# Performance work log

Hardware: AMD Instinct MI355X
Metric: run time of the kernel (lower is better)

Reference implementation:

```python
import jax, jax.numpy as jnp
import numpy as np

D_MODEL = 768
NUM_HEADS = 12
HEAD_DIM = D_MODEL // NUM_HEADS
BATCH = 1
SEQ = 4096


def setup_inputs() -> dict:
    key = jax.random.key(0)
    ks = jax.random.split(key, 11)
    s = 0.02
    return {
        "q": jax.random.normal(ks[0], (BATCH, SEQ, D_MODEL), jnp.float32),
        "k": jax.random.normal(ks[1], (BATCH, SEQ, D_MODEL), jnp.float32),
        "v": jax.random.normal(ks[2], (BATCH, SEQ, D_MODEL), jnp.float32),
        "Wq": jax.random.normal(ks[3], (D_MODEL, D_MODEL), jnp.float32) * s,
        "bq": jnp.zeros((D_MODEL,), jnp.float32),
        "Wk": jax.random.normal(ks[4], (D_MODEL, D_MODEL), jnp.float32) * s,
        "bk": jnp.zeros((D_MODEL,), jnp.float32),
        "Wv": jax.random.normal(ks[5], (D_MODEL, D_MODEL), jnp.float32) * s,
        "bv": jnp.zeros((D_MODEL,), jnp.float32),
        "Wo": jax.random.normal(ks[6], (D_MODEL, D_MODEL), jnp.float32) * s,
        "bo": jnp.zeros((D_MODEL,), jnp.float32),
    }


def reference(q, k, v, Wq, bq, Wk, bk, Wv, bv, Wo, bo):
    B, S, D = q.shape
    H, Hd = NUM_HEADS, HEAD_DIM
    # linear projections (torch Linear: x @ W.T + b)
    qh = (q @ Wq.T + bq).reshape(B, S, H, Hd).transpose(0, 2, 1, 3)  # [B,H,S,Hd]
    kh = (k @ Wk.T + bk).reshape(B, S, H, Hd).transpose(0, 2, 1, 3)
    vh = (v @ Wv.T + bv).reshape(B, S, H, Hd).transpose(0, 2, 1, 3)
    scale = 1.0 / jnp.sqrt(jnp.asarray(Hd, qh.dtype))
    scores = jnp.einsum("bhsd,bhtd->bhst", qh, kh) * scale  # [B,H,S,S]
    weights = jax.nn.softmax(scores, axis=-1)
    attn = jnp.einsum("bhst,bhtd->bhsd", weights, vh)  # [B,H,S,Hd]
    attn = attn.transpose(0, 2, 1, 3).reshape(B, S, D)
    return attn @ Wo.T + bo
```

## Files before the change

### kernel.cpp

```cpp
#include <hip/hip_runtime.h>

#define S_LEN 4096
#define DMODEL 768
#define NHEAD 12
#define HD 64

typedef __bf16 bf16x8 __attribute__((ext_vector_type(8)));
typedef __bf16 bf16x4 __attribute__((ext_vector_type(4)));
typedef float f32x4 __attribute__((ext_vector_type(4)));
typedef float f32x16 __attribute__((ext_vector_type(16)));
typedef unsigned short u16x8 __attribute__((ext_vector_type(8)));
typedef unsigned short u16x4 __attribute__((ext_vector_type(4)));
typedef _Float16 f16x4 __attribute__((ext_vector_type(4)));

#if __has_builtin(__builtin_amdgcn_exp2f)
#define EXP2F(x) __builtin_amdgcn_exp2f(x)
#else
#define EXP2F(x) exp2f(x)
#endif

#define MFMA32(a, b, c) __builtin_amdgcn_mfma_f32_32x32x16_bf16(a, b, c, 0, 0, 0)

__device__ __forceinline__ unsigned short f2bf(float f) {
  unsigned int u = __float_as_uint(f);
  u += 0x7fffu + ((u >> 16) & 1u);
  return (unsigned short)(u >> 16);
}

__device__ __forceinline__ void gload_lds16(const void* g, void* l) {
  __builtin_amdgcn_global_load_lds(
      (__attribute__((address_space(1))) void*)g,
      (__attribute__((address_space(3))) void*)l, 16, 0, 0);
}

struct CvtArgs {
  const float* src[7];
  unsigned short* dst[7];
  int n[7];
};

__global__ __launch_bounds__(256) void cvt_kernel(CvtArgs a) {
  const int seg = blockIdx.y;
  const int n = a.n[seg];
  const int i = (blockIdx.x * 256 + threadIdx.x) * 8;
  if (i >= n) return;
  const float* s = a.src[seg] + i;
  u16x8 o;
#pragma unroll
  for (int j = 0; j < 8; ++j) o[j] = f2bf(s[j]);
  *reinterpret_cast<u16x8*>(a.dst[seg] + i) = o;
}

struct QkvArgs {
  const unsigned short* A[3];
  const unsigned short* W[3];
  const float* bias[3];
  unsigned short* dst[3];
  float scale[3];
};

__global__ __launch_bounds__(256) void qkv_gemm(QkvArgs a) {
  __shared__ unsigned char lds[32768];
  const int z = blockIdx.z;
  const unsigned short* __restrict__ A = a.A[z];
  const unsigned short* __restrict__ B = a.W[z];
  const float* __restrict__ bias = a.bias[z];
  unsigned short* __restrict__ dst = a.dst[z];
  const float scale = a.scale[z];

  const int tid = threadIdx.x;
  const int lane = tid & 63;
  const int w = tid >> 6;
  const int wr = w >> 1, wc = w & 1;
  const int c = lane & 15, g = lane >> 4;
  const int m0 = blockIdx.x * 128;
  const int n0 = blockIdx.y * 128;

  f32x4 acc[4][4] = {};

  for (int kt = 0; kt < DMODEL / 64; ++kt) {
#pragma unroll
    for (int p = 0; p < 4; ++p) {
      const int te = p * 256 + tid;
      const int row = te >> 3;
      const int sb = ((te & 7) * 16) ^ ((row & 7) << 4);
      gload_lds16(A + (size_t)(m0 + row) * DMODEL + kt * 64 + (sb >> 1), &lds[te * 16]);
      gload_lds16(B + (size_t)(n0 + row) * DMODEL + kt * 64 + (sb >> 1), &lds[16384 + te * 16]);
    }
    __syncthreads();

    bf16x8 af[4][2], bfr[4][2];
#pragma unroll
    for (int mb = 0; mb < 4; ++mb)
#pragma unroll
      for (int ks = 0; ks < 2; ++ks) {
        const int row = wr * 64 + mb * 16 + c;
        const int byte = (ks * 64 + g * 16) ^ ((row & 7) << 4);
        af[mb][ks] = *reinterpret_cast<const bf16x8*>(&lds[row * 128 + byte]);
      }
#pragma unroll
    for (int nb = 0; nb < 4; ++nb)
#pragma unroll
      for (int ks = 0; ks < 2; ++ks) {
        const int row = wc * 64 + nb * 16 + c;
        const int byte = (ks * 64 + g * 16) ^ ((row & 7) << 4);
        bfr[nb][ks] = *reinterpret_cast<const bf16x8*>(&lds[16384 + row * 128 + byte]);
      }
    __builtin_amdgcn_s_setprio(1);
#pragma unroll
    for (int ks = 0; ks < 2; ++ks)
#pragma unroll
      for (int mb = 0; mb < 4; ++mb)
#pragma unroll
        for (int nb = 0; nb < 4; ++nb)
          acc[mb][nb] = __builtin_amdgcn_mfma_f32_16x16x32_bf16(
              af[mb][ks], bfr[nb][ks], acc[mb][nb], 0, 0, 0);
    __builtin_amdgcn_s_setprio(0);
    __syncthreads();
  }

#pragma unroll
  for (int mb = 0; mb < 4; ++mb) {
#pragma unroll
    for (int nb = 0; nb < 4; ++nb) {
      const int n = n0 + wc * 64 + nb * 16 + c;
      const float bv = bias[n];
#pragma unroll
      for (int r = 0; r < 4; ++r) {
        const int m = m0 + wr * 64 + mb * 16 + g * 4 + r;
        const float v = (acc[mb][nb][r] + bv) * scale;
        const int hh = n >> 6, hd = n & 63;
        if (z != 2) {
          dst[((size_t)hh * S_LEN + m) * HD + hd] = f2bf(v);
        } else {
          const int mp = (m & ~12) | ((m & 4) << 1) | ((m & 8) >> 1);
          dst[((size_t)hh * HD + hd) * S_LEN + mp] = f2bf(v);
        }
      }
    }
  }
}

__global__ __launch_bounds__(256) void gemm_out(
    const unsigned short* __restrict__ A, const unsigned short* __restrict__ B,
    const float* __restrict__ bias, float* __restrict__ dst) {
  __shared__ unsigned char lds[32768];
  const int tid = threadIdx.x;
  const int lane = tid & 63;
  const int w = tid >> 6;
  const int wr = w >> 1, wc = w & 1;
  const int c = lane & 15, g = lane >> 4;
  const int m0 = blockIdx.x * 128;
  const int n0 = blockIdx.y * 128;

  f32x4 acc[4][4] = {};

  for (int kt = 0; kt < DMODEL / 64; ++kt) {
#pragma unroll
    for (int p = 0; p < 4; ++p) {
      const int te = p * 256 + tid;
      const int row = te >> 3;
      const int sb = ((te & 7) * 16) ^ ((row & 7) << 4);
      gload_lds16(A + (size_t)(m0 + row) * DMODEL + kt * 64 + (sb >> 1), &lds[te * 16]);
      gload_lds16(B + (size_t)(n0 + row) * DMODEL + kt * 64 + (sb >> 1), &lds[16384 + te * 16]);
    }
    __syncthreads();

    bf16x8 af[4][2], bfr[4][2];
#pragma unroll
    for (int mb = 0; mb < 4; ++mb)
#pragma unroll
      for (int ks = 0; ks < 2; ++ks) {
        const int row = wr * 64 + mb * 16 + c;
        const int byte = (ks * 64 + g * 16) ^ ((row & 7) << 4);
        af[mb][ks] = *reinterpret_cast<const bf16x8*>(&lds[row * 128 + byte]);
      }
#pragma unroll
    for (int nb = 0; nb < 4; ++nb)
#pragma unroll
      for (int ks = 0; ks < 2; ++ks) {
        const int row = wc * 64 + nb * 16 + c;
        const int byte = (ks * 64 + g * 16) ^ ((row & 7) << 4);
        bfr[nb][ks] = *reinterpret_cast<const bf16x8*>(&lds[16384 + row * 128 + byte]);
      }
    __builtin_amdgcn_s_setprio(1);
#pragma unroll
    for (int ks = 0; ks < 2; ++ks)
#pragma unroll
      for (int mb = 0; mb < 4; ++mb)
#pragma unroll
        for (int nb = 0; nb < 4; ++nb)
          acc[mb][nb] = __builtin_amdgcn_mfma_f32_16x16x32_bf16(
              af[mb][ks], bfr[nb][ks], acc[mb][nb], 0, 0, 0);
    __builtin_amdgcn_s_setprio(0);
    __syncthreads();
  }

#pragma unroll
  for (int mb = 0; mb < 4; ++mb)
#pragma unroll
    for (int nb = 0; nb < 4; ++nb) {
      const int n = n0 + wc * 64 + nb * 16 + c;
      const float bv = bias[n];
#pragma unroll
      for (int r = 0; r < 4; ++r) {
        const int m = m0 + wr * 64 + mb * 16 + g * 4 + r;
        dst[(size_t)m * DMODEL + n] = acc[mb][nb][r] + bv;
      }
    }
}

__global__ __launch_bounds__(256) void attn_kernel(
    const unsigned short* __restrict__ qh,
    const unsigned short* __restrict__ kh,
    const unsigned short* __restrict__ vtp,
    _Float16* __restrict__ pacc,
    float* __restrict__ prs) {
  __shared__ unsigned char lds[32768];
  const int tid = threadIdx.x;
  const int lane = tid & 63;
  const int w = tid >> 6;
  const int c5 = lane & 31;
  const int h2 = lane >> 5;
  const int hh = blockIdx.y;
  const int split = blockIdx.z;
  const int qw = blockIdx.x * 128 + w * 32;
  const int kv0 = split * (S_LEN / 2);
  const int NKT = (S_LEN / 2) / 64;

  bf16x8 qa[4];
#pragma unroll
  for (int ks = 0; ks < 4; ++ks)
    qa[ks] = *reinterpret_cast<const bf16x8*>(
        qh + ((size_t)hh * S_LEN + qw + c5) * HD + ks * 16 + h2 * 8);

  const int r63 = tid & 63;
  const int kch = tid >> 6;
  const unsigned short* ksrc =
      kh + ((size_t)hh * S_LEN + kv0 + r63) * HD + kch * 8;
  const unsigned short* vsrc =
      vtp + ((size_t)hh * HD + r63) * S_LEN + kv0 + kch * 8;
  const int dL = tid * 16;

  gload_lds16(ksrc, &lds[dL]);
  gload_lds16(ksrc + 32, &lds[4096 + dL]);
  gload_lds16(vsrc, &lds[8192 + dL]);
  gload_lds16(vsrc + 32, &lds[12288 + dL]);
  ksrc += 64 * HD;
  vsrc += 64;

  f32x16 accO[2] = {};
  float rs0 = 0.f, rs1 = 0.f, rs2 = 0.f, rs3 = 0.f;

  auto compute = [&](const unsigned char* Kb, const unsigned char* Vb) {
    f32x16 s0 = {}, s1 = {};
    __builtin_amdgcn_s_setprio(1);
#pragma unroll
    for (int ks = 0; ks < 4; ++ks) {
      const unsigned char* kbase = Kb + (ks * 2 + h2) * 1024 + c5 * 16;
      const bf16x8 k0 = *reinterpret_cast<const bf16x8*>(kbase);
      const bf16x8 k1 = *reinterpret_cast<const bf16x8*>(kbase + 512);
      s0 = MFMA32(k0, qa[ks], s0);
      s1 = MFMA32(k1, qa[ks], s1);
    }
    __builtin_amdgcn_s_setprio(0);

    bf16x8 p00, p01, p10, p11;
#pragma unroll
    for (int r = 0; r < 8; ++r) {
      const float e0 = EXP2F(s0[r]);
      const float e1 = EXP2F(s0[8 + r]);
      const float e2 = EXP2F(s1[r]);
      const float e3 = EXP2F(s1[8 + r]);
      rs0 += e0; rs1 += e1; rs2 += e2; rs3 += e3;
      p00[r] = (__bf16)e0;
      p01[r] = (__bf16)e1;
      p10[r] = (__bf16)e2;
      p11[r] = (__bf16)e3;
    }

    __builtin_amdgcn_s_setprio(1);
#pragma unroll
    for (int t = 0; t < 2; ++t)
#pragma unroll
      for (int ss = 0; ss < 2; ++ss) {
        const bf16x8 pb = t ? (ss ? p11 : p10) : (ss ? p01 : p00);
        const unsigned char* vbase = Vb + (t * 4 + ss * 2 + h2) * 1024 + c5 * 16;
        const bf16x8 va0 = *reinterpret_cast<const bf16x8*>(vbase);
        const bf16x8 va1 = *reinterpret_cast<const bf16x8*>(vbase + 512);
        accO[0] = MFMA32(va0, pb, accO[0]);
        accO[1] = MFMA32(va1, pb, accO[1]);
      }
    __builtin_amdgcn_s_setprio(0);
  };

  int buf = 0;
  for (int kt = 0; kt < NKT - 1; ++kt) {
    const int nb_ = (buf ^ 1) * 16384;
    gload_lds16(ksrc, &lds[nb_ + dL]);
    gload_lds16(ksrc + 32, &lds[nb_ + 4096 + dL]);
    gload_lds16(vsrc, &lds[nb_ + 8192 + dL]);
    gload_lds16(vsrc + 32, &lds[nb_ + 12288 + dL]);
    ksrc += 64 * HD;
    vsrc += 64;
    asm volatile("s_waitcnt vmcnt(4)" ::: "memory");
    __builtin_amdgcn_sched_barrier(0);
    __builtin_amdgcn_s_barrier();
    __builtin_amdgcn_sched_barrier(0);
    compute(&lds[buf * 16384], &lds[buf * 16384 + 8192]);
    asm volatile("s_waitcnt lgkmcnt(0)" ::: "memory");
    __builtin_amdgcn_sched_barrier(0);
    __builtin_amdgcn_s_barrier();
    buf ^= 1;
  }
  asm volatile("s_waitcnt vmcnt(0)" ::: "memory");
  __builtin_amdgcn_sched_barrier(0);
  __builtin_amdgcn_s_barrier();
  __builtin_amdgcn_sched_barrier(0);
  compute(&lds[buf * 16384], &lds[buf * 16384 + 8192]);

  float rsA = (rs0 + rs1) + (rs2 + rs3);
  rsA += __shfl_xor(rsA, 32);
  const size_t hqbase = ((size_t)split * NHEAD + hh) * S_LEN + qw + c5;
  if (h2 == 0) prs[hqbase] = rsA * 0.015625f;
#pragma unroll
  for (int dt = 0; dt < 2; ++dt)
#pragma unroll
    for (int rr = 0; rr < 4; ++rr) {
      f16x4 o;
#pragma unroll
      for (int j = 0; j < 4; ++j)
        o[j] = (_Float16)(accO[dt][rr * 4 + j] * 0.015625f);
      *reinterpret_cast<f16x4*>(
          pacc + hqbase * 64 + dt * 32 + rr * 8 + h2 * 4) = o;
    }
}

__global__ __launch_bounds__(256) void combine_kernel(
    const _Float16* __restrict__ pacc, const float* __restrict__ prs,
    unsigned short* __restrict__ attb) {
  const int idx = blockIdx.x * 256 + threadIdx.x;
  const int hq = idx >> 4;
  const int d4 = (idx & 15) * 4;
  const int h = hq >> 12;
  const int q = hq & 4095;
  const size_t o0 = (size_t)hq * 64 + d4;
  const size_t o1 = o0 + (size_t)NHEAD * S_LEN * 64;
  const f16x4 av = *reinterpret_cast<const f16x4*>(pacc + o0);
  const f16x4 bv = *reinterpret_cast<const f16x4*>(pacc + o1);
  const float inv = 1.f / (prs[hq] + prs[hq + NHEAD * S_LEN]);
  u16x4 ov;
#pragma unroll
  for (int j = 0; j < 4; ++j)
    ov[j] = f2bf(((float)av[j] + (float)bv[j]) * inv);
  *reinterpret_cast<u16x4*>(attb + (size_t)q * DMODEL + h * HD + d4) = ov;
}

extern "C" void kernel_launch(void* const* d_in, const int* in_sizes, int n_in,
                              void* d_out, int out_size, void* d_ws, size_t ws_size,
                              hipStream_t stream) {
  (void)in_sizes; (void)n_in; (void)out_size;
  const float* q  = (const float*)d_in[0];
  const float* k  = (const float*)d_in[1];
  const float* v  = (const float*)d_in[2];
  const float* Wq = (const float*)d_in[3];
  const float* bq = (const float*)d_in[4];
  const float* Wk = (const float*)d_in[5];
  const float* bk = (const float*)d_in[6];
  const float* Wv = (const float*)d_in[7];
  const float* bv = (const float*)d_in[8];
  const float* Wo = (const float*)d_in[9];
  const float* bo = (const float*)d_in[10];
  float* out = (float*)d_out;

  const size_t SD = (size_t)S_LEN * DMODEL;
  const size_t DD = (size_t)DMODEL * DMODEL;
  if (ws_size < (7 * SD + 4 * DD) * 2) return;

  unsigned short* ws   = (unsigned short*)d_ws;
  unsigned short* qbf  = ws;
  unsigned short* kbf  = qbf + SD;
  unsigned short* vbf  = kbf + SD;
  unsigned short* wqb  = vbf + SD;
  unsigned short* wkb  = wqb + DD;
  unsigned short* wvb  = wkb + DD;
  unsigned short* wob  = wvb + DD;
  unsigned short* qhb  = wob + DD;
  unsigned short* khb  = qhb + SD;
  unsigned short* vtb  = khb + SD;
  unsigned short* attb = vtb + SD;

  _Float16* pacc = (_Float16*)qbf;
  float*    prs  = (float*)wqb;

  CvtArgs ca;
  ca.src[0] = q;  ca.dst[0] = qbf; ca.n[0] = (int)SD;
  ca.src[1] = k;  ca.dst[1] = kbf; ca.n[1] = (int)SD;
  ca.src[2] = v;  ca.dst[2] = vbf; ca.n[2] = (int)SD;
  ca.src[3] = Wq; ca.dst[3] = wqb; ca.n[3] = (int)DD;
  ca.src[4] = Wk; ca.dst[4] = wkb; ca.n[4] = (int)DD;
  ca.src[5] = Wv; ca.dst[5] = wvb; ca.n[5] = (int)DD;
  ca.src[6] = Wo; ca.dst[6] = wob; ca.n[6] = (int)DD;
  cvt_kernel<<<dim3(1536, 7), 256, 0, stream>>>(ca);

  QkvArgs qa;
  qa.A[0] = qbf; qa.W[0] = wqb; qa.bias[0] = bq; qa.dst[0] = qhb;
  qa.scale[0] = 0.18033688011112042f;
  qa.A[1] = kbf; qa.W[1] = wkb; qa.bias[1] = bk; qa.dst[1] = khb;
  qa.scale[1] = 1.0f;
  qa.A[2] = vbf; qa.W[2] = wvb; qa.bias[2] = bv; qa.dst[2] = vtb;
  qa.scale[2] = 1.0f;
  qkv_gemm<<<dim3(32, 6, 3), 256, 0, stream>>>(qa);

  attn_kernel<<<dim3(S_LEN / 128, NHEAD, 2), 256, 0, stream>>>(
      qhb, khb, vtb, pacc, prs);

  combine_kernel<<<dim3((NHEAD * S_LEN * 16) / 256), 256, 0, stream>>>(
      pacc, prs, attb);

  gemm_out<<<dim3(32, 6), 256, 0, stream>>>(attb, wob, bo, out);
}
```

Baseline: 136.5 us.

## Triple-buffer K/V tiles with one barrier per step and interleave exp with PV MFMAs

The attention loop moves from double to triple buffering of K/V tiles in LDS, prefetching two tiles ahead. This allows a single workgroup barrier per iteration instead of two. The exp/bf16 conversion of scores is also split per 8-element chunk and interleaved with the PV MFMAs, so exp work for one chunk can overlap with matrix ops of another. The LDS allocation grows from 32 KB to 48 KB per block, which may reduce how many blocks fit on each CU.

```diff
diff --git a/kernel.cpp b/kernel.cpp
--- a/kernel.cpp
+++ b/kernel.cpp
@@ -216,7 +216,7 @@
     const unsigned short* __restrict__ vtp,
     _Float16* __restrict__ pacc,
     float* __restrict__ prs) {
-  __shared__ unsigned char lds[32768];
+  __shared__ unsigned char lds[49152];
   const int tid = threadIdx.x;
   const int lane = tid & 63;
   const int w = tid >> 6;
@@ -235,19 +235,23 @@
         qh + ((size_t)hh * S_LEN + qw + c5) * HD + ks * 16 + h2 * 8);
 
   const int r63 = tid & 63;
-  const int kch = tid >> 6;
   const unsigned short* ksrc =
-      kh + ((size_t)hh * S_LEN + kv0 + r63) * HD + kch * 8;
+      kh + ((size_t)hh * S_LEN + kv0 + r63) * HD + (tid >> 6) * 8;
   const unsigned short* vsrc =
-      vtp + ((size_t)hh * HD + r63) * S_LEN + kv0 + kch * 8;
+      vtp + ((size_t)hh * HD + r63) * S_LEN + kv0 + (tid >> 6) * 8;
   const int dL = tid * 16;
 
-  gload_lds16(ksrc, &lds[dL]);
-  gload_lds16(ksrc + 32, &lds[4096 + dL]);
-  gload_lds16(vsrc, &lds[8192 + dL]);
-  gload_lds16(vsrc + 32, &lds[12288 + dL]);
-  ksrc += 64 * HD;
-  vsrc += 64;
+  auto stage = [&](int bo) {
+    gload_lds16(ksrc, &lds[bo + dL]);
+    gload_lds16(ksrc + 32, &lds[bo + 4096 + dL]);
+    gload_lds16(vsrc, &lds[bo + 8192 + dL]);
+    gload_lds16(vsrc + 32, &lds[bo + 12288 + dL]);
+    ksrc += 64 * HD;
+    vsrc += 64;
+  };
+
+  stage(0);
+  stage(16384);
 
   f32x16 accO[2] = {};
   float rs0 = 0.f, rs1 = 0.f, rs2 = 0.f, rs3 = 0.f;
@@ -265,59 +269,54 @@
     }
     __builtin_amdgcn_s_setprio(0);
 
-    bf16x8 p00, p01, p10, p11;
-#pragma unroll
-    for (int r = 0; r < 8; ++r) {
-      const float e0 = EXP2F(s0[r]);
-      const float e1 = EXP2F(s0[8 + r]);
-      const float e2 = EXP2F(s1[r]);
-      const float e3 = EXP2F(s1[8 + r]);
-      rs0 += e0; rs1 += e1; rs2 += e2; rs3 += e3;
-      p00[r] = (__bf16)e0;
-      p01[r] = (__bf16)e1;
-      p10[r] = (__bf16)e2;
-      p11[r] = (__bf16)e3;
-    }
-
-    __builtin_amdgcn_s_setprio(1);
 #pragma unroll
     for (int t = 0; t < 2; ++t)
 #pragma unroll
       for (int ss = 0; ss < 2; ++ss) {
-        const bf16x8 pb = t ? (ss ? p11 : p10) : (ss ? p01 : p00);
         const unsigned char* vbase = Vb + (t * 4 + ss * 2 + h2) * 1024 + c5 * 16;
         const bf16x8 va0 = *reinterpret_cast<const bf16x8*>(vbase);
         const bf16x8 va1 = *reinterpret_cast<const bf16x8*>(vbase + 512);
+        bf16x8 pb;
+        float racc = 0.f;
+#pragma unroll
+        for (int r = 0; r < 8; ++r) {
+          const float e = EXP2F(t ? s1[ss * 8 + r] : s0[ss * 8 + r]);
+          racc += e;
+          pb[r] = (__bf16)e;
+        }
+        if (t == 0) { if (ss == 0) rs0 += racc; else rs1 += racc; }
+        else        { if (ss == 0) rs2 += racc; else rs3 += racc; }
+        __builtin_amdgcn_s_setprio(1);
         accO[0] = MFMA32(va0, pb, accO[0]);
         accO[1] = MFMA32(va1, pb, accO[1]);
-      }
-    __builtin_amdgcn_s_setprio(0);
+        __builtin_amdgcn_s_setprio(0);
+      }
   };
 
-  int buf = 0;
-  for (int kt = 0; kt < NKT - 1; ++kt) {
-    const int nb_ = (buf ^ 1) * 16384;
-    gload_lds16(ksrc, &lds[nb_ + dL]);
-    gload_lds16(ksrc + 32, &lds[nb_ + 4096 + dL]);
-    gload_lds16(vsrc, &lds[nb_ + 8192 + dL]);
-    gload_lds16(vsrc + 32, &lds[nb_ + 12288 + dL]);
-    ksrc += 64 * HD;
-    vsrc += 64;
-    asm volatile("s_waitcnt vmcnt(4)" ::: "memory");
-    __builtin_amdgcn_sched_barrier(0);
-    __builtin_amdgcn_s_barrier();
-    __builtin_amdgcn_sched_barrier(0);
-    compute(&lds[buf * 16384], &lds[buf * 16384 + 8192]);
-    asm volatile("s_waitcnt lgkmcnt(0)" ::: "memory");
-    __builtin_amdgcn_sched_barrier(0);
-    __builtin_amdgcn_s_barrier();
-    buf ^= 1;
+  int boC = 0;
+  int boS = 32768;
+  for (int t = 0; t < NKT; ++t) {
+    if (t + 2 < NKT) {
+      asm volatile("s_waitcnt vmcnt(4)" ::: "memory");
+      __builtin_amdgcn_sched_barrier(0);
+      __builtin_amdgcn_s_barrier();
+      __builtin_amdgcn_sched_barrier(0);
+      stage(boS);
+    } else if (t + 1 < NKT) {
+      asm volatile("s_waitcnt vmcnt(4)" ::: "memory");
+      __builtin_amdgcn_sched_barrier(0);
+      __builtin_amdgcn_s_barrier();
+      __builtin_amdgcn_sched_barrier(0);
+    } else {
+      asm volatile("s_waitcnt vmcnt(0)" ::: "memory");
+      __builtin_amdgcn_sched_barrier(0);
+      __builtin_amdgcn_s_barrier();
+      __builtin_amdgcn_sched_barrier(0);
+    }
+    compute(&lds[boC], &lds[boC + 8192]);
+    boC += 16384; if (boC == 49152) boC = 0;
+    boS += 16384; if (boS == 49152) boS = 0;
   }
-  asm volatile("s_waitcnt vmcnt(0)" ::: "memory");
-  __builtin_amdgcn_sched_barrier(0);
-  __builtin_amdgcn_s_barrier();
-  __builtin_amdgcn_sched_barrier(0);
-  compute(&lds[buf * 16384], &lds[buf * 16384 + 8192]);
 
   float rsA = (rs0 + rs1) + (rs2 + rs3);
   rsA += __shfl_xor(rsA, 32);
```

New measurement: 127.5 us. 6.5% less time.
